# Performance work log

Hardware: AMD Instinct MI355X
Metric: run time of the kernel (lower is better)

The kernel has to match this reference:

```python
import jax, jax.numpy as jnp
import numpy as np

INPUT_SIZE = 24
HIDDEN = 128
N_LAYERS = 2
OUT_SIZE = 1


def setup_inputs() -> dict:
    key = jax.random.key(0)
    ks = jax.random.split(key, 2 + 4 * N_LAYERS + 2)
    x = jax.random.normal(ks[0], (2048, 128, INPUT_SIZE), dtype=jnp.float32)
    params = {}
    s = 1.0 / np.sqrt(HIDDEN)
    idx = 1
    for l in range(N_LAYERS):
        in_dim = INPUT_SIZE if l == 0 else HIDDEN
        params[f"W_ih{l}"] = jax.random.uniform(ks[idx], (4 * HIDDEN, in_dim), minval=-s, maxval=s, dtype=jnp.float32); idx += 1
        params[f"W_hh{l}"] = jax.random.uniform(ks[idx], (4 * HIDDEN, HIDDEN), minval=-s, maxval=s, dtype=jnp.float32); idx += 1
        params[f"b_ih{l}"] = jax.random.uniform(ks[idx], (4 * HIDDEN,), minval=-s, maxval=s, dtype=jnp.float32); idx += 1
        params[f"b_hh{l}"] = jax.random.uniform(ks[idx], (4 * HIDDEN,), minval=-s, maxval=s, dtype=jnp.float32); idx += 1
    params["W_fc"] = jax.random.uniform(ks[idx], (OUT_SIZE, HIDDEN), minval=-s, maxval=s, dtype=jnp.float32); idx += 1
    params["b_fc"] = jax.random.uniform(ks[idx], (OUT_SIZE,), minval=-s, maxval=s, dtype=jnp.float32)
    return {"x": x, **params}


def _lstm_layer(x, W_ih, W_hh, b_ih, b_hh):
    # x: [B, T, in] -> outputs [B, T, H]. PyTorch gate order: i, f, g, o.
    B = x.shape[0]
    H = W_hh.shape[1]
    # precompute input projections for all timesteps: [T, B, 4H]
    xproj = jnp.einsum('bti,gi->tbg', x, W_ih) + b_ih + b_hh

    def step(carry, xp_t):
        h, c = carry
        gates = xp_t + h @ W_hh.T  # [B, 4H]
        i, f, g, o = jnp.split(gates, 4, axis=-1)
        i = jax.nn.sigmoid(i)
        f = jax.nn.sigmoid(f)
        g = jnp.tanh(g)
        o = jax.nn.sigmoid(o)
        c = f * c + i * g
        h = o * jnp.tanh(c)
        return (h, c), h

    h0 = jnp.zeros((B, H), dtype=x.dtype)
    c0 = jnp.zeros((B, H), dtype=x.dtype)
    (_, _), hs = jax.lax.scan(step, (h0, c0), xproj)
    return jnp.transpose(hs, (1, 0, 2))  # [B, T, H]


def reference(x, W_ih0, W_hh0, b_ih0, b_hh0, W_ih1, W_hh1, b_ih1, b_hh1, W_fc, b_fc):
    # Inference-mode forward: inter-layer dropout (p=0.2) is identity in eval.
    h1 = _lstm_layer(x, W_ih0, W_hh0, b_ih0, b_hh0)   # [B, T, H]
    h2 = _lstm_layer(h1, W_ih1, W_hh1, b_ih1, b_hh1)  # [B, T, H]
    last = h2[:, -1, :]                               # [B, H]
    return last @ W_fc.T + b_fc                       # [B, 1]
```

## Files before the change

### kernel.cpp

```cpp
#include <hip/hip_runtime.h>

#define TSTEPS 128
#define NIN 24
#define HD 128
#define NG 512
#define BT 16
#define NBLK 128
#define NTH 512

#define S0 168
#define S1 264
#define X0COLS 32
#define H1COL 128

typedef _Float16 half8  __attribute__((ext_vector_type(8)));
typedef _Float16 half4v __attribute__((ext_vector_type(4)));
typedef float    floatx4 __attribute__((ext_vector_type(4)));

__device__ __forceinline__ float sigf(float x) {
    return __builtin_amdgcn_rcpf(1.0f + __expf(-x));
}
__device__ __forceinline__ float tanh_f(float x) {
    return 1.0f - 2.0f * __builtin_amdgcn_rcpf(1.0f + __expf(2.0f * x));
}

__device__ __forceinline__ half8 ldw8(const float* p) {
    const float4* q = (const float4*)p;
    float4 a = q[0], b = q[1];
    half8 r;
    r[0] = (_Float16)a.x; r[1] = (_Float16)a.y; r[2] = (_Float16)a.z; r[3] = (_Float16)a.w;
    r[4] = (_Float16)b.x; r[5] = (_Float16)b.y; r[6] = (_Float16)b.z; r[7] = (_Float16)b.w;
    return r;
}

__global__ __launch_bounds__(NTH, 2)
void lstm2_fused(const float* __restrict__ x,
                 const float* __restrict__ Wih0, const float* __restrict__ Whh0,
                 const float* __restrict__ bih0, const float* __restrict__ bhh0,
                 const float* __restrict__ Wih1, const float* __restrict__ Whh1,
                 const float* __restrict__ bih1, const float* __restrict__ bhh1,
                 const float* __restrict__ Wfc,  const float* __restrict__ bfc,
                 float* __restrict__ out, _Float16* __restrict__ h1ws)
{
    __shared__ _Float16 A0[2][BT * S0];
    __shared__ _Float16 A1[2][BT * S1];

    const int tid = threadIdx.x;
    const int blk = blockIdx.x;
    const int wv  = tid >> 6;
    const int ln  = tid & 63;
    const int qd  = ln >> 4;
    const int nn  = ln & 15;
    const int b0  = blk * BT;

    for (int i = tid; i < BT * S0; i += NTH) { A0[0][i] = (_Float16)0.f; A0[1][i] = (_Float16)0.f; }
    for (int i = tid; i < BT * S1; i += NTH) { A1[0][i] = (_Float16)0.f; A1[1][i] = (_Float16)0.f; }

    float bias0[4], bias1[4];
#pragma unroll
    for (int tI = 0; tI < 4; ++tI) {
        int g = tI * HD + wv * 16 + nn;
        bias0[tI] = bih0[g] + bhh0[g];
        bias1[tI] = bih1[g] + bhh1[g];
    }

    half8 w0[4][5];
#pragma unroll
    for (int tI = 0; tI < 4; ++tI) {
        int g = tI * HD + wv * 16 + nn;
        if (qd < 3) w0[tI][0] = ldw8(Wih0 + g * NIN + qd * 8);
        else        { half8 z = {0,0,0,0,0,0,0,0}; w0[tI][0] = z; }
#pragma unroll
        for (int kk = 1; kk < 5; ++kk)
            w0[tI][kk] = ldw8(Whh0 + g * HD + (kk - 1) * 32 + qd * 8);
    }

    __syncthreads();

    if (tid < BT * NIN) {
        int m = tid / NIN, c = tid % NIN;
        A0[0][m * S0 + c] = (_Float16)x[(size_t)(b0 + m) * (TSTEPS * NIN) + c];
    }

    float cs[4] = {0.f, 0.f, 0.f, 0.f};

#pragma unroll 1
    for (int t = 0; t < TSTEPS; ++t) {
        const int cur = t & 1, nxt = cur ^ 1;
        __syncthreads();

        if (t > 0) {
            int m = tid >> 5, c4 = (tid & 31) * 4;
            half4v v = *(const half4v*)&A0[cur][m * S0 + X0COLS + c4];
            *(half4v*)(h1ws + ((size_t)((t - 1) * NBLK + blk) * BT + m) * HD + c4) = v;
        }
        if (t + 1 < TSTEPS && tid < BT * NIN) {
            int m = tid / NIN, c = tid % NIN;
            A0[nxt][m * S0 + c] = (_Float16)x[(size_t)(b0 + m) * (TSTEPS * NIN) + (t + 1) * NIN + c];
        }

        half8 af[5];
#pragma unroll
        for (int kk = 0; kk < 5; ++kk)
            af[kk] = *(const half8*)&A0[cur][nn * S0 + kk * 32 + qd * 8];

        floatx4 acc[4];
#pragma unroll
        for (int tI = 0; tI < 4; ++tI) {
            floatx4 a = {bias0[tI], bias0[tI], bias0[tI], bias0[tI]};
#pragma unroll
            for (int kk = 0; kk < 5; ++kk)
                a = __builtin_amdgcn_mfma_f32_16x16x32_f16(af[kk], w0[tI][kk], a, 0, 0, 0);
            acc[tI] = a;
        }

        const int jc = X0COLS + wv * 16 + nn;
#pragma unroll
        for (int r = 0; r < 4; ++r) {
            float iv = sigf(acc[0][r]);
            float fv = sigf(acc[1][r]);
            float gv = tanh_f(acc[2][r]);
            float ov = sigf(acc[3][r]);
            float cn = fv * cs[r] + iv * gv;
            cs[r] = cn;
            float hv = ov * tanh_f(cn);
            A0[nxt][(qd * 4 + r) * S0 + jc] = (_Float16)hv;
        }
    }
    __syncthreads();
    {
        int m = tid >> 5, c4 = (tid & 31) * 4;
        half4v v = *(const half4v*)&A0[0][m * S0 + X0COLS + c4];
        *(half4v*)(h1ws + ((size_t)(127 * NBLK + blk) * BT + m) * HD + c4) = v;
    }

    half8 w1[4][8];
#pragma unroll
    for (int tI = 0; tI < 4; ++tI) {
        int g = tI * HD + wv * 16 + nn;
#pragma unroll
        for (int kk = 0; kk < 4; ++kk)
            w1[tI][kk] = ldw8(Wih1 + g * HD + kk * 32 + qd * 8);
#pragma unroll
        for (int kk = 4; kk < 8; ++kk)
            w1[tI][kk] = ldw8(Whh1 + g * HD + (kk - 4) * 32 + qd * 8);
    }
    {
        int m = tid >> 5, c4 = (tid & 31) * 4;
        half4v v = *(const half4v*)(h1ws + ((size_t)blk * BT + m) * HD + c4);
        *(half4v*)&A1[0][m * S1 + c4] = v;
    }
    float cs1[4] = {0.f, 0.f, 0.f, 0.f};

#pragma unroll 1
    for (int t = 0; t < TSTEPS; ++t) {
        const int cur = t & 1, nxt = cur ^ 1;
        __syncthreads();

        int m = tid >> 5, c4 = (tid & 31) * 4;
        half4v pre;
        if (t + 1 < TSTEPS)
            pre = *(const half4v*)(h1ws + ((size_t)((t + 1) * NBLK + blk) * BT + m) * HD + c4);

        half8 af[8];
#pragma unroll
        for (int kk = 0; kk < 8; ++kk)
            af[kk] = *(const half8*)&A1[cur][nn * S1 + kk * 32 + qd * 8];

        floatx4 acc[4];
#pragma unroll
        for (int tI = 0; tI < 4; ++tI) {
            floatx4 a = {bias1[tI], bias1[tI], bias1[tI], bias1[tI]};
#pragma unroll
            for (int kk = 0; kk < 8; ++kk)
                a = __builtin_amdgcn_mfma_f32_16x16x32_f16(af[kk], w1[tI][kk], a, 0, 0, 0);
            acc[tI] = a;
        }

        const int jc = H1COL + wv * 16 + nn;
#pragma unroll
        for (int r = 0; r < 4; ++r) {
            float iv = sigf(acc[0][r]);
            float fv = sigf(acc[1][r]);
            float gv = tanh_f(acc[2][r]);
            float ov = sigf(acc[3][r]);
            float cn = fv * cs1[r] + iv * gv;
            cs1[r] = cn;
            float hv = ov * tanh_f(cn);
            A1[nxt][(qd * 4 + r) * S1 + jc] = (_Float16)hv;
        }
        if (t + 1 < TSTEPS)
            *(half4v*)&A1[nxt][m * S1 + c4] = pre;
    }
    __syncthreads();

    {
        int b = tid >> 5, sub = tid & 31;
        const _Float16* hp = &A1[0][b * S1 + H1COL + sub * 4];
        const float4 wv4 = *(const float4*)(Wfc + sub * 4);
        float s = (float)hp[0] * wv4.x + (float)hp[1] * wv4.y
                + (float)hp[2] * wv4.z + (float)hp[3] * wv4.w;
        s += __shfl_down(s, 16, 32);
        s += __shfl_down(s, 8, 32);
        s += __shfl_down(s, 4, 32);
        s += __shfl_down(s, 2, 32);
        s += __shfl_down(s, 1, 32);
        if (sub == 0) out[b0 + b] = s + bfc[0];
    }
}

extern "C" void kernel_launch(void* const* d_in, const int* in_sizes, int n_in,
                              void* d_out, int out_size, void* d_ws, size_t ws_size,
                              hipStream_t stream) {
    const float* x    = (const float*)d_in[0];
    const float* Wih0 = (const float*)d_in[1];
    const float* Whh0 = (const float*)d_in[2];
    const float* bih0 = (const float*)d_in[3];
    const float* bhh0 = (const float*)d_in[4];
    const float* Wih1 = (const float*)d_in[5];
    const float* Whh1 = (const float*)d_in[6];
    const float* bih1 = (const float*)d_in[7];
    const float* bhh1 = (const float*)d_in[8];
    const float* Wfc  = (const float*)d_in[9];
    const float* bfc  = (const float*)d_in[10];
    float* out = (float*)d_out;
    _Float16* h1ws = (_Float16*)d_ws;

    lstm2_fused<<<dim3(NBLK), dim3(NTH), 0, stream>>>(
        x, Wih0, Whh0, bih0, bhh0, Wih1, Whh1, bih1, bhh1, Wfc, bfc, out, h1ws);
}
```

Measured before the change: 390.9 us.

## Batch x loads and h1 workspace traffic into multi-step chunks via LDS ring

Rewrites the shared memory layout: layer-0 hidden states go into a 9-slot LDS ring and are flushed to the workspace in 8-timestep chunks, and x is loaded 8 steps at a time with float4 reads into a double buffer. Layer 1 prefetches 4 timesteps of h1 per chunk into LDS instead of one per step. The workspace layout becomes per-block contiguous. The goal is to take per-step global latency off the serial recurrence, at the cost of more LDS and bursty chunk work every few steps.

```diff
diff --git a/kernel.cpp b/kernel.cpp
--- a/kernel.cpp
+++ b/kernel.cpp
@@ -3,15 +3,23 @@
 #define TSTEPS 128
 #define NIN 24
 #define HD 128
-#define NG 512
 #define BT 16
 #define NBLK 128
 #define NTH 512
 
-#define S0 168
-#define S1 264
-#define X0COLS 32
-#define H1COL 128
+#define RS    136
+#define SLOT  (BT*RS)
+#define XS    40
+#define XTS   (BT*XS)
+#define XBUF  (8*XTS)
+#define RINGN 9
+
+#define RING_OFF 0
+#define XB_OFF   (RINGN*SLOT)
+#define SM_SIZE  (XB_OFF + 2*XBUF)
+
+#define HB_OFF 0
+#define B2_OFF (8*SLOT)
 
 typedef _Float16 half8  __attribute__((ext_vector_type(8)));
 typedef _Float16 half4v __attribute__((ext_vector_type(4)));
@@ -42,8 +50,7 @@
                  const float* __restrict__ Wfc,  const float* __restrict__ bfc,
                  float* __restrict__ out, _Float16* __restrict__ h1ws)
 {
-    __shared__ _Float16 A0[2][BT * S0];
-    __shared__ _Float16 A1[2][BT * S1];
+    __shared__ __align__(16) _Float16 SM[SM_SIZE];
 
     const int tid = threadIdx.x;
     const int blk = blockIdx.x;
@@ -52,9 +59,11 @@
     const int qd  = ln >> 4;
     const int nn  = ln & 15;
     const int b0  = blk * BT;
-
-    for (int i = tid; i < BT * S0; i += NTH) { A0[0][i] = (_Float16)0.f; A0[1][i] = (_Float16)0.f; }
-    for (int i = tid; i < BT * S1; i += NTH) { A1[0][i] = (_Float16)0.f; A1[1][i] = (_Float16)0.f; }
+    const size_t wsbase = (size_t)blk * (TSTEPS * BT * HD);
+
+    const half8 z8 = {0, 0, 0, 0, 0, 0, 0, 0};
+
+    for (int i = tid * 8; i < SM_SIZE; i += NTH * 8) *(half8*)&SM[i] = z8;
 
     float bias0[4], bias1[4];
 #pragma unroll
@@ -64,120 +73,187 @@
         bias1[tI] = bih1[g] + bhh1[g];
     }
 
-    half8 w0[4][5];
+    half8 wih0[4];
+    half8 whh0[4][4];
 #pragma unroll
     for (int tI = 0; tI < 4; ++tI) {
         int g = tI * HD + wv * 16 + nn;
-        if (qd < 3) w0[tI][0] = ldw8(Wih0 + g * NIN + qd * 8);
-        else        { half8 z = {0,0,0,0,0,0,0,0}; w0[tI][0] = z; }
-#pragma unroll
-        for (int kk = 1; kk < 5; ++kk)
-            w0[tI][kk] = ldw8(Whh0 + g * HD + (kk - 1) * 32 + qd * 8);
+        if (qd < 3) wih0[tI] = ldw8(Wih0 + g * NIN + qd * 8);
+        else        wih0[tI] = z8;
+#pragma unroll
+        for (int kk = 0; kk < 4; ++kk)
+            whh0[tI][kk] = ldw8(Whh0 + g * HD + kk * 32 + qd * 8);
     }
 
     __syncthreads();
 
-    if (tid < BT * NIN) {
-        int m = tid / NIN, c = tid % NIN;
-        A0[0][m * S0 + c] = (_Float16)x[(size_t)(b0 + m) * (TSTEPS * NIN) + c];
-    }
-
-    float cs[4] = {0.f, 0.f, 0.f, 0.f};
+    {
+        const int c = 0, buf = 0;
+        for (int i = tid; i < 8 * BT * 6; i += NTH) {
+            int ti = i / 96, r = i % 96, b = r / 6, q = r % 6;
+            float4 v = *(const float4*)(x + (size_t)(b0 + b) * (TSTEPS * NIN)
+                                          + (size_t)(c * 8 + ti) * NIN + q * 4);
+            half4v h; h[0] = (_Float16)v.x; h[1] = (_Float16)v.y;
+                      h[2] = (_Float16)v.z; h[3] = (_Float16)v.w;
+            *(half4v*)&SM[XB_OFF + buf * XBUF + ti * XTS + b * XS + q * 4] = h;
+        }
+    }
+
+    float cs0[4] = {0.f, 0.f, 0.f, 0.f};
+    const int jc = wv * 16 + nn;
 
 #pragma unroll 1
     for (int t = 0; t < TSTEPS; ++t) {
-        const int cur = t & 1, nxt = cur ^ 1;
         __syncthreads();
 
-        if (t > 0) {
-            int m = tid >> 5, c4 = (tid & 31) * 4;
-            half4v v = *(const half4v*)&A0[cur][m * S0 + X0COLS + c4];
-            *(half4v*)(h1ws + ((size_t)((t - 1) * NBLK + blk) * BT + m) * HD + c4) = v;
-        }
-        if (t + 1 < TSTEPS && tid < BT * NIN) {
-            int m = tid / NIN, c = tid % NIN;
-            A0[nxt][m * S0 + c] = (_Float16)x[(size_t)(b0 + m) * (TSTEPS * NIN) + (t + 1) * NIN + c];
-        }
-
-        half8 af[5];
-#pragma unroll
-        for (int kk = 0; kk < 5; ++kk)
-            af[kk] = *(const half8*)&A0[cur][nn * S0 + kk * 32 + qd * 8];
+        if ((t & 7) == 0) {
+            if (t + 8 < TSTEPS) {
+                const int c = (t >> 3) + 1, buf = c & 1;
+                for (int i = tid; i < 8 * BT * 6; i += NTH) {
+                    int ti = i / 96, r = i % 96, b = r / 6, q = r % 6;
+                    float4 v = *(const float4*)(x + (size_t)(b0 + b) * (TSTEPS * NIN)
+                                                  + (size_t)(c * 8 + ti) * NIN + q * 4);
+                    half4v h; h[0] = (_Float16)v.x; h[1] = (_Float16)v.y;
+                              h[2] = (_Float16)v.z; h[3] = (_Float16)v.w;
+                    *(half4v*)&SM[XB_OFF + buf * XBUF + ti * XTS + b * XS + q * 4] = h;
+                }
+            }
+            if (t > 0) {
+                const int c = (t >> 3) - 1;
+#pragma unroll
+                for (int k = 0; k < 4; ++k) {
+                    int e  = tid + k * NTH;
+                    int ti = e >> 8;
+                    int r  = e & 255;
+                    int b  = r >> 4;
+                    int c8 = (r & 15) * 8;
+                    int tau = c * 8 + ti;
+                    half8 v = *(const half8*)&SM[RING_OFF + (tau % 9) * SLOT + b * RS + c8];
+                    *(half8*)(h1ws + wsbase + ((size_t)tau * BT + b) * HD + c8) = v;
+                }
+            }
+        }
+
+        const half8 ax = *(const half8*)&SM[XB_OFF + ((t >> 3) & 1) * XBUF
+                                            + (t & 7) * XTS + nn * XS + qd * 8];
+        const int sprev = (t + 8) % 9;
+        half8 ah[4];
+#pragma unroll
+        for (int kk = 0; kk < 4; ++kk)
+            ah[kk] = *(const half8*)&SM[RING_OFF + sprev * SLOT + nn * RS + kk * 32 + qd * 8];
 
         floatx4 acc[4];
 #pragma unroll
         for (int tI = 0; tI < 4; ++tI) {
             floatx4 a = {bias0[tI], bias0[tI], bias0[tI], bias0[tI]};
-#pragma unroll
-            for (int kk = 0; kk < 5; ++kk)
-                a = __builtin_amdgcn_mfma_f32_16x16x32_f16(af[kk], w0[tI][kk], a, 0, 0, 0);
+            a = __builtin_amdgcn_mfma_f32_16x16x32_f16(ax, wih0[tI], a, 0, 0, 0);
+#pragma unroll
+            for (int kk = 0; kk < 4; ++kk)
+                a = __builtin_amdgcn_mfma_f32_16x16x32_f16(ah[kk], whh0[tI][kk], a, 0, 0, 0);
             acc[tI] = a;
         }
 
-        const int jc = X0COLS + wv * 16 + nn;
+        const int scur = t % 9;
 #pragma unroll
         for (int r = 0; r < 4; ++r) {
             float iv = sigf(acc[0][r]);
             float fv = sigf(acc[1][r]);
             float gv = tanh_f(acc[2][r]);
             float ov = sigf(acc[3][r]);
-            float cn = fv * cs[r] + iv * gv;
-            cs[r] = cn;
+            float cn = fv * cs0[r] + iv * gv;
+            cs0[r] = cn;
             float hv = ov * tanh_f(cn);
-            A0[nxt][(qd * 4 + r) * S0 + jc] = (_Float16)hv;
-        }
-    }
+            SM[RING_OFF + scur * SLOT + (qd * 4 + r) * RS + jc] = (_Float16)hv;
+        }
+    }
+
     __syncthreads();
     {
-        int m = tid >> 5, c4 = (tid & 31) * 4;
-        half4v v = *(const half4v*)&A0[0][m * S0 + X0COLS + c4];
-        *(half4v*)(h1ws + ((size_t)(127 * NBLK + blk) * BT + m) * HD + c4) = v;
-    }
-
-    half8 w1[4][8];
+        const int c = 15;
+#pragma unroll
+        for (int k = 0; k < 4; ++k) {
+            int e  = tid + k * NTH;
+            int ti = e >> 8;
+            int r  = e & 255;
+            int b  = r >> 4;
+            int c8 = (r & 15) * 8;
+            int tau = c * 8 + ti;
+            half8 v = *(const half8*)&SM[RING_OFF + (tau % 9) * SLOT + b * RS + c8];
+            *(half8*)(h1ws + wsbase + ((size_t)tau * BT + b) * HD + c8) = v;
+        }
+    }
+
+    half8 wih1[4][4], whh1[4][4];
 #pragma unroll
     for (int tI = 0; tI < 4; ++tI) {
         int g = tI * HD + wv * 16 + nn;
 #pragma unroll
-        for (int kk = 0; kk < 4; ++kk)
-            w1[tI][kk] = ldw8(Wih1 + g * HD + kk * 32 + qd * 8);
-#pragma unroll
-        for (int kk = 4; kk < 8; ++kk)
-            w1[tI][kk] = ldw8(Whh1 + g * HD + (kk - 4) * 32 + qd * 8);
-    }
+        for (int kk = 0; kk < 4; ++kk) {
+            wih1[tI][kk] = ldw8(Wih1 + g * HD + kk * 32 + qd * 8);
+            whh1[tI][kk] = ldw8(Whh1 + g * HD + kk * 32 + qd * 8);
+        }
+    }
+
+    __syncthreads();
+
+    for (int i = tid * 8; i < 2 * SLOT; i += NTH * 8) *(half8*)&SM[B2_OFF + i] = z8;
     {
-        int m = tid >> 5, c4 = (tid & 31) * 4;
-        half4v v = *(const half4v*)(h1ws + ((size_t)blk * BT + m) * HD + c4);
-        *(half4v*)&A1[0][m * S1 + c4] = v;
-    }
+        const int c = 0, buf = 0;
+#pragma unroll
+        for (int k = 0; k < 2; ++k) {
+            int e  = tid + k * NTH;
+            int ti = e >> 8;
+            int r  = e & 255;
+            int b  = r >> 4;
+            int c8 = (r & 15) * 8;
+            half8 v = *(const half8*)(h1ws + wsbase + ((size_t)(c * 4 + ti) * BT + b) * HD + c8);
+            *(half8*)&SM[HB_OFF + buf * (4 * SLOT) + ti * SLOT + b * RS + c8] = v;
+        }
+    }
+
     float cs1[4] = {0.f, 0.f, 0.f, 0.f};
 
 #pragma unroll 1
-    for (int t = 0; t < TSTEPS; ++t) {
-        const int cur = t & 1, nxt = cur ^ 1;
+    for (int tau = 0; tau < TSTEPS; ++tau) {
         __syncthreads();
 
-        int m = tid >> 5, c4 = (tid & 31) * 4;
-        half4v pre;
-        if (t + 1 < TSTEPS)
-            pre = *(const half4v*)(h1ws + ((size_t)((t + 1) * NBLK + blk) * BT + m) * HD + c4);
-
-        half8 af[8];
-#pragma unroll
-        for (int kk = 0; kk < 8; ++kk)
-            af[kk] = *(const half8*)&A1[cur][nn * S1 + kk * 32 + qd * 8];
+        if ((tau & 3) == 0 && tau + 4 < TSTEPS) {
+            const int c = (tau >> 2) + 1, buf = c & 1;
+#pragma unroll
+            for (int k = 0; k < 2; ++k) {
+                int e  = tid + k * NTH;
+                int ti = e >> 8;
+                int r  = e & 255;
+                int b  = r >> 4;
+                int c8 = (r & 15) * 8;
+                half8 v = *(const half8*)(h1ws + wsbase + ((size_t)(c * 4 + ti) * BT + b) * HD + c8);
+                *(half8*)&SM[HB_OFF + buf * (4 * SLOT) + ti * SLOT + b * RS + c8] = v;
+            }
+        }
+
+        const int cur = tau & 1, nxt = cur ^ 1;
+        const int hbase = HB_OFF + ((tau >> 2) & 1) * (4 * SLOT) + (tau & 3) * SLOT;
+
+        half8 a1[4], a2[4];
+#pragma unroll
+        for (int kk = 0; kk < 4; ++kk) {
+            a1[kk] = *(const half8*)&SM[hbase + nn * RS + kk * 32 + qd * 8];
+            a2[kk] = *(const half8*)&SM[B2_OFF + cur * SLOT + nn * RS + kk * 32 + qd * 8];
+        }
 
         floatx4 acc[4];
 #pragma unroll
         for (int tI = 0; tI < 4; ++tI) {
             floatx4 a = {bias1[tI], bias1[tI], bias1[tI], bias1[tI]};
 #pragma unroll
-            for (int kk = 0; kk < 8; ++kk)
-                a = __builtin_amdgcn_mfma_f32_16x16x32_f16(af[kk], w1[tI][kk], a, 0, 0, 0);
+            for (int kk = 0; kk < 4; ++kk)
+                a = __builtin_amdgcn_mfma_f32_16x16x32_f16(a1[kk], wih1[tI][kk], a, 0, 0, 0);
+#pragma unroll
+            for (int kk = 0; kk < 4; ++kk)
+                a = __builtin_amdgcn_mfma_f32_16x16x32_f16(a2[kk], whh1[tI][kk], a, 0, 0, 0);
             acc[tI] = a;
         }
 
-        const int jc = H1COL + wv * 16 + nn;
 #pragma unroll
         for (int r = 0; r < 4; ++r) {
             float iv = sigf(acc[0][r]);
@@ -187,16 +263,14 @@
             float cn = fv * cs1[r] + iv * gv;
             cs1[r] = cn;
             float hv = ov * tanh_f(cn);
-            A1[nxt][(qd * 4 + r) * S1 + jc] = (_Float16)hv;
-        }
-        if (t + 1 < TSTEPS)
-            *(half4v*)&A1[nxt][m * S1 + c4] = pre;
+            SM[B2_OFF + nxt * SLOT + (qd * 4 + r) * RS + jc] = (_Float16)hv;
+        }
     }
     __syncthreads();
 
     {
         int b = tid >> 5, sub = tid & 31;
-        const _Float16* hp = &A1[0][b * S1 + H1COL + sub * 4];
+        const _Float16* hp = &SM[B2_OFF + b * RS + sub * 4];
         const float4 wv4 = *(const float4*)(Wfc + sub * 4);
         float s = (float)hp[0] * wv4.x + (float)hp[1] * wv4.y
                 + (float)hp[2] * wv4.z + (float)hp[3] * wv4.w;
```

New measurement: 371.5 us. 1.05x faster.

## Interleave both LSTM layers in one wavefront-skewed time loop

Applied to the files above, without the earlier changes.

Runs layer 0 at step t and layer 1 at step t-1 inside a single 129-iteration loop, so the two recurrences share each barrier and the layer-0 hidden states stay in LDS instead of going through a global workspace. Input x is prefetched four timesteps at a time into double-buffered LDS chunks. The W_ih0 fragments, with the layer-0 bias folded in through a constant-1 input column, are moved to LDS to free registers for holding both layers' weights at once. This removes one full sequential 128-step pass and the workspace round-trip, at the cost of higher register pressure and longer per-step work.

```diff
diff --git a/kernel.cpp b/kernel.cpp
--- a/kernel.cpp
+++ b/kernel.cpp
@@ -3,15 +3,22 @@
 #define TSTEPS 128
 #define NIN 24
 #define HD 128
-#define NG 512
 #define BT 16
 #define NBLK 128
 #define NTH 512
 
-#define S0 168
-#define S1 264
-#define X0COLS 32
-#define H1COL 128
+#define RS    136
+#define SLOT  (BT*RS)
+#define XS    40
+#define XTS   (BT*XS)
+#define XCH   4
+#define XBUF  (XCH*XTS)
+
+#define WIH0_OFF 0
+#define H1_OFF   16384
+#define H2_OFF   (H1_OFF + 2*SLOT)
+#define XB_OFF   (H2_OFF + 2*SLOT)
+#define SM_SIZE  (XB_OFF + 2*XBUF)
 
 typedef _Float16 half8  __attribute__((ext_vector_type(8)));
 typedef _Float16 half4v __attribute__((ext_vector_type(4)));
@@ -34,16 +41,15 @@
 }
 
 __global__ __launch_bounds__(NTH, 2)
-void lstm2_fused(const float* __restrict__ x,
-                 const float* __restrict__ Wih0, const float* __restrict__ Whh0,
-                 const float* __restrict__ bih0, const float* __restrict__ bhh0,
-                 const float* __restrict__ Wih1, const float* __restrict__ Whh1,
-                 const float* __restrict__ bih1, const float* __restrict__ bhh1,
-                 const float* __restrict__ Wfc,  const float* __restrict__ bfc,
-                 float* __restrict__ out, _Float16* __restrict__ h1ws)
+void lstm2_il(const float* __restrict__ x,
+              const float* __restrict__ Wih0, const float* __restrict__ Whh0,
+              const float* __restrict__ bih0, const float* __restrict__ bhh0,
+              const float* __restrict__ Wih1, const float* __restrict__ Whh1,
+              const float* __restrict__ bih1, const float* __restrict__ bhh1,
+              const float* __restrict__ Wfc,  const float* __restrict__ bfc,
+              float* __restrict__ out)
 {
-    __shared__ _Float16 A0[2][BT * S0];
-    __shared__ _Float16 A1[2][BT * S1];
+    __shared__ __align__(16) _Float16 SM[SM_SIZE];
 
     const int tid = threadIdx.x;
     const int blk = blockIdx.x;
@@ -52,151 +58,157 @@
     const int qd  = ln >> 4;
     const int nn  = ln & 15;
     const int b0  = blk * BT;
-
-    for (int i = tid; i < BT * S0; i += NTH) { A0[0][i] = (_Float16)0.f; A0[1][i] = (_Float16)0.f; }
-    for (int i = tid; i < BT * S1; i += NTH) { A1[0][i] = (_Float16)0.f; A1[1][i] = (_Float16)0.f; }
-
-    float bias0[4], bias1[4];
+    const int jc  = wv * 16 + nn;
+
+    const half8 z8 = {0, 0, 0, 0, 0, 0, 0, 0};
+
+    for (int i = tid * 8; i < SM_SIZE; i += NTH * 8) *(half8*)&SM[i] = z8;
+
+    half8 whh0[4][4];
+    half8 w1[4][8];
+    float bias1[4];
 #pragma unroll
     for (int tI = 0; tI < 4; ++tI) {
         int g = tI * HD + wv * 16 + nn;
-        bias0[tI] = bih0[g] + bhh0[g];
         bias1[tI] = bih1[g] + bhh1[g];
-    }
-
-    half8 w0[4][5];
-#pragma unroll
-    for (int tI = 0; tI < 4; ++tI) {
-        int g = tI * HD + wv * 16 + nn;
-        if (qd < 3) w0[tI][0] = ldw8(Wih0 + g * NIN + qd * 8);
-        else        { half8 z = {0,0,0,0,0,0,0,0}; w0[tI][0] = z; }
-#pragma unroll
-        for (int kk = 1; kk < 5; ++kk)
-            w0[tI][kk] = ldw8(Whh0 + g * HD + (kk - 1) * 32 + qd * 8);
+#pragma unroll
+        for (int kk = 0; kk < 4; ++kk) {
+            whh0[tI][kk] = ldw8(Whh0 + g * HD + kk * 32 + qd * 8);
+            w1[tI][kk]     = ldw8(Wih1 + g * HD + kk * 32 + qd * 8);
+            w1[tI][4 + kk] = ldw8(Whh1 + g * HD + kk * 32 + qd * 8);
+        }
+    }
+
+    for (int e = tid; e < 2048; e += NTH) {
+        int tI2 = e >> 9, wv2 = (e >> 6) & 7, ln2 = e & 63;
+        int qd2 = ln2 >> 4, nn2 = ln2 & 15;
+        int g = tI2 * HD + wv2 * 16 + nn2;
+        half8 f = z8;
+        if (qd2 < 3) f = ldw8(Wih0 + g * NIN + qd2 * 8);
+        else         f[0] = (_Float16)(bih0[g] + bhh0[g]);
+        *(half8*)&SM[WIH0_OFF + e * 8] = f;
     }
 
     __syncthreads();
 
-    if (tid < BT * NIN) {
-        int m = tid / NIN, c = tid % NIN;
-        A0[0][m * S0 + c] = (_Float16)x[(size_t)(b0 + m) * (TSTEPS * NIN) + c];
-    }
-
-    float cs[4] = {0.f, 0.f, 0.f, 0.f};
+    if (tid < XCH * BT * 7) {
+        int ti = tid / 112, r = tid % 112, b = r / 7, q = r % 7;
+        half4v h;
+        if (q < 6) {
+            float4 v = *(const float4*)(x + (size_t)(b0 + b) * (TSTEPS * NIN) + ti * NIN + q * 4);
+            h[0] = (_Float16)v.x; h[1] = (_Float16)v.y; h[2] = (_Float16)v.z; h[3] = (_Float16)v.w;
+        } else {
+            h[0] = (_Float16)1.f; h[1] = 0; h[2] = 0; h[3] = 0;
+        }
+        *(half4v*)&SM[XB_OFF + ti * XTS + b * XS + q * 4] = h;
+    }
+
+    float cs0[4] = {0.f, 0.f, 0.f, 0.f};
+    float cs1[4] = {0.f, 0.f, 0.f, 0.f};
 
 #pragma unroll 1
-    for (int t = 0; t < TSTEPS; ++t) {
-        const int cur = t & 1, nxt = cur ^ 1;
+    for (int t = 0; t <= TSTEPS; ++t) {
         __syncthreads();
 
-        if (t > 0) {
-            int m = tid >> 5, c4 = (tid & 31) * 4;
-            half4v v = *(const half4v*)&A0[cur][m * S0 + X0COLS + c4];
-            *(half4v*)(h1ws + ((size_t)((t - 1) * NBLK + blk) * BT + m) * HD + c4) = v;
-        }
-        if (t + 1 < TSTEPS && tid < BT * NIN) {
-            int m = tid / NIN, c = tid % NIN;
-            A0[nxt][m * S0 + c] = (_Float16)x[(size_t)(b0 + m) * (TSTEPS * NIN) + (t + 1) * NIN + c];
-        }
-
-        half8 af[5];
-#pragma unroll
-        for (int kk = 0; kk < 5; ++kk)
-            af[kk] = *(const half8*)&A0[cur][nn * S0 + kk * 32 + qd * 8];
-
-        floatx4 acc[4];
-#pragma unroll
-        for (int tI = 0; tI < 4; ++tI) {
-            floatx4 a = {bias0[tI], bias0[tI], bias0[tI], bias0[tI]};
-#pragma unroll
-            for (int kk = 0; kk < 5; ++kk)
-                a = __builtin_amdgcn_mfma_f32_16x16x32_f16(af[kk], w0[tI][kk], a, 0, 0, 0);
-            acc[tI] = a;
-        }
-
-        const int jc = X0COLS + wv * 16 + nn;
-#pragma unroll
-        for (int r = 0; r < 4; ++r) {
-            float iv = sigf(acc[0][r]);
-            float fv = sigf(acc[1][r]);
-            float gv = tanh_f(acc[2][r]);
-            float ov = sigf(acc[3][r]);
-            float cn = fv * cs[r] + iv * gv;
-            cs[r] = cn;
-            float hv = ov * tanh_f(cn);
-            A0[nxt][(qd * 4 + r) * S0 + jc] = (_Float16)hv;
-        }
-    }
-    __syncthreads();
-    {
-        int m = tid >> 5, c4 = (tid & 31) * 4;
-        half4v v = *(const half4v*)&A0[0][m * S0 + X0COLS + c4];
-        *(half4v*)(h1ws + ((size_t)(127 * NBLK + blk) * BT + m) * HD + c4) = v;
-    }
-
-    half8 w1[4][8];
-#pragma unroll
-    for (int tI = 0; tI < 4; ++tI) {
-        int g = tI * HD + wv * 16 + nn;
-#pragma unroll
-        for (int kk = 0; kk < 4; ++kk)
-            w1[tI][kk] = ldw8(Wih1 + g * HD + kk * 32 + qd * 8);
-#pragma unroll
-        for (int kk = 4; kk < 8; ++kk)
-            w1[tI][kk] = ldw8(Whh1 + g * HD + (kk - 4) * 32 + qd * 8);
-    }
-    {
-        int m = tid >> 5, c4 = (tid & 31) * 4;
-        half4v v = *(const half4v*)(h1ws + ((size_t)blk * BT + m) * HD + c4);
-        *(half4v*)&A1[0][m * S1 + c4] = v;
-    }
-    float cs1[4] = {0.f, 0.f, 0.f, 0.f};
-
-#pragma unroll 1
-    for (int t = 0; t < TSTEPS; ++t) {
-        const int cur = t & 1, nxt = cur ^ 1;
-        __syncthreads();
-
-        int m = tid >> 5, c4 = (tid & 31) * 4;
-        half4v pre;
-        if (t + 1 < TSTEPS)
-            pre = *(const half4v*)(h1ws + ((size_t)((t + 1) * NBLK + blk) * BT + m) * HD + c4);
-
-        half8 af[8];
-#pragma unroll
-        for (int kk = 0; kk < 8; ++kk)
-            af[kk] = *(const half8*)&A1[cur][nn * S1 + kk * 32 + qd * 8];
-
-        floatx4 acc[4];
-#pragma unroll
-        for (int tI = 0; tI < 4; ++tI) {
-            floatx4 a = {bias1[tI], bias1[tI], bias1[tI], bias1[tI]};
-#pragma unroll
-            for (int kk = 0; kk < 8; ++kk)
-                a = __builtin_amdgcn_mfma_f32_16x16x32_f16(af[kk], w1[tI][kk], a, 0, 0, 0);
-            acc[tI] = a;
-        }
-
-        const int jc = H1COL + wv * 16 + nn;
-#pragma unroll
-        for (int r = 0; r < 4; ++r) {
-            float iv = sigf(acc[0][r]);
-            float fv = sigf(acc[1][r]);
-            float gv = tanh_f(acc[2][r]);
-            float ov = sigf(acc[3][r]);
-            float cn = fv * cs1[r] + iv * gv;
-            cs1[r] = cn;
-            float hv = ov * tanh_f(cn);
-            A1[nxt][(qd * 4 + r) * S1 + jc] = (_Float16)hv;
-        }
-        if (t + 1 < TSTEPS)
-            *(half4v*)&A1[nxt][m * S1 + c4] = pre;
+        if (t < TSTEPS && (t & (XCH - 1)) == 0 && t + XCH < TSTEPS) {
+            const int c = (t >> 2) + 1, buf = c & 1;
+            if (tid < XCH * BT * 7) {
+                int ti = tid / 112, r = tid % 112, b = r / 7, q = r % 7;
+                half4v h;
+                if (q < 6) {
+                    float4 v = *(const float4*)(x + (size_t)(b0 + b) * (TSTEPS * NIN)
+                                                  + (size_t)(c * XCH + ti) * NIN + q * 4);
+                    h[0] = (_Float16)v.x; h[1] = (_Float16)v.y;
+                    h[2] = (_Float16)v.z; h[3] = (_Float16)v.w;
+                } else {
+                    h[0] = (_Float16)1.f; h[1] = 0; h[2] = 0; h[3] = 0;
+                }
+                *(half4v*)&SM[XB_OFF + buf * XBUF + ti * XTS + b * XS + q * 4] = h;
+            }
+        }
+
+        if (t < TSTEPS) {
+            const half8 ax = *(const half8*)&SM[XB_OFF + ((t >> 2) & 1) * XBUF
+                                                + (t & (XCH - 1)) * XTS + nn * XS + qd * 8];
+            floatx4 acc[4];
+#pragma unroll
+            for (int tI = 0; tI < 4; ++tI) {
+                const half8 wf = *(const half8*)&SM[WIH0_OFF + ((tI * 8 + wv) * 64 + ln) * 8];
+                floatx4 a = {0.f, 0.f, 0.f, 0.f};
+                acc[tI] = __builtin_amdgcn_mfma_f32_16x16x32_f16(ax, wf, a, 0, 0, 0);
+            }
+            const int rp = (t & 1) ^ 1;
+            half8 ah[4];
+#pragma unroll
+            for (int kk = 0; kk < 4; ++kk)
+                ah[kk] = *(const half8*)&SM[H1_OFF + rp * SLOT + nn * RS + kk * 32 + qd * 8];
+#pragma unroll
+            for (int tI = 0; tI < 4; ++tI) {
+#pragma unroll
+                for (int kk = 0; kk < 4; ++kk)
+                    acc[tI] = __builtin_amdgcn_mfma_f32_16x16x32_f16(ah[kk], whh0[tI][kk], acc[tI], 0, 0, 0);
+            }
+            const int wp = t & 1;
+#pragma unroll
+            for (int r = 0; r < 4; ++r) {
+                float iv = sigf(acc[0][r]);
+                float fv = sigf(acc[1][r]);
+                float gv = tanh_f(acc[2][r]);
+                float ov = sigf(acc[3][r]);
+                float cn = fv * cs0[r] + iv * gv;
+                cs0[r] = cn;
+                float hv = ov * tanh_f(cn);
+                SM[H1_OFF + wp * SLOT + (qd * 4 + r) * RS + jc] = (_Float16)hv;
+            }
+        }
+
+        if (t >= 1) {
+            const int rp = (t & 1) ^ 1;
+            floatx4 acc[4];
+#pragma unroll
+            for (int tI = 0; tI < 4; ++tI) {
+                floatx4 a = {bias1[tI], bias1[tI], bias1[tI], bias1[tI]};
+                acc[tI] = a;
+            }
+            half8 a1[4];
+#pragma unroll
+            for (int kk = 0; kk < 4; ++kk)
+                a1[kk] = *(const half8*)&SM[H1_OFF + rp * SLOT + nn * RS + kk * 32 + qd * 8];
+#pragma unroll
+            for (int tI = 0; tI < 4; ++tI) {
+#pragma unroll
+                for (int kk = 0; kk < 4; ++kk)
+                    acc[tI] = __builtin_amdgcn_mfma_f32_16x16x32_f16(a1[kk], w1[tI][kk], acc[tI], 0, 0, 0);
+            }
+            half8 a2[4];
+#pragma unroll
+            for (int kk = 0; kk < 4; ++kk)
+                a2[kk] = *(const half8*)&SM[H2_OFF + (t & 1) * SLOT + nn * RS + kk * 32 + qd * 8];
+#pragma unroll
+            for (int tI = 0; tI < 4; ++tI) {
+#pragma unroll
+                for (int kk = 0; kk < 4; ++kk)
+                    acc[tI] = __builtin_amdgcn_mfma_f32_16x16x32_f16(a2[kk], w1[tI][4 + kk], acc[tI], 0, 0, 0);
+            }
+            const int wp = (t & 1) ^ 1;
+#pragma unroll
+            for (int r = 0; r < 4; ++r) {
+                float iv = sigf(acc[0][r]);
+                float fv = sigf(acc[1][r]);
+                float gv = tanh_f(acc[2][r]);
+                float ov = sigf(acc[3][r]);
+                float cn = fv * cs1[r] + iv * gv;
+                cs1[r] = cn;
+                float hv = ov * tanh_f(cn);
+                SM[H2_OFF + wp * SLOT + (qd * 4 + r) * RS + jc] = (_Float16)hv;
+            }
+        }
     }
     __syncthreads();
 
     {
         int b = tid >> 5, sub = tid & 31;
-        const _Float16* hp = &A1[0][b * S1 + H1COL + sub * 4];
+        const _Float16* hp = &SM[H2_OFF + SLOT + b * RS + sub * 4];
         const float4 wv4 = *(const float4*)(Wfc + sub * 4);
         float s = (float)hp[0] * wv4.x + (float)hp[1] * wv4.y
                 + (float)hp[2] * wv4.z + (float)hp[3] * wv4.w;
@@ -224,8 +236,7 @@
     const float* Wfc  = (const float*)d_in[9];
     const float* bfc  = (const float*)d_in[10];
     float* out = (float*)d_out;
-    _Float16* h1ws = (_Float16*)d_ws;
-
-    lstm2_fused<<<dim3(NBLK), dim3(NTH), 0, stream>>>(
-        x, Wih0, Whh0, bih0, bhh0, Wih1, Whh1, bih1, bhh1, Wfc, bfc, out, h1ws);
-}
+
+    lstm2_il<<<dim3(NBLK), dim3(NTH), 0, stream>>>(
+        x, Wih0, Whh0, bih0, bhh0, Wih1, Whh1, bih1, bhh1, Wfc, bfc, out);
+}
```

New measurement: 473.4 us. 21.1% more time.
